# Optimization experiments

Hardware: AMD Instinct MI355X
Metric: run time of the kernel (lower is better)

The kernel has to match this reference:

```python
import jax, jax.numpy as jnp
import numpy as np

V, E_DIM, HID, GNN_O, HEADS = 50257, 256, 128, 128, 4
N_NODES, N_EDGES, T_LEN = 10000, 160000, 64
NEG_SLOPE = 0.2


def gatv2(x, src, dst, Wl, Wr, att, bias, concat):
    """PyG GATv2Conv (share_weights=False, self-loops already in src/dst)."""
    heads, out_ch = att.shape
    n = x.shape[0]
    xl = (x @ Wl).reshape(n, heads, out_ch)   # source transform
    xr = (x @ Wr).reshape(n, heads, out_ch)   # target transform
    e = jax.nn.leaky_relu(xl[src] + xr[dst], NEG_SLOPE)        # [E, h, c]
    logits = jnp.einsum('ehc,hc->eh', e, att)                  # [E, h]
    m = jax.ops.segment_max(logits, dst, num_segments=n)
    a = jnp.exp(logits - m[dst])
    a = a / jax.ops.segment_sum(a, dst, num_segments=n)[dst]
    out = jax.ops.segment_sum(xl[src] * a[..., None], dst, num_segments=n)
    out = out.reshape(n, heads * out_ch) if concat else out.mean(axis=1)
    return out + bias


def setup_inputs() -> dict:
    key = jax.random.key(0)
    ks = jax.random.split(key, 16)
    g = lambda k, shape: jax.random.normal(k, shape, jnp.float32) * 0.05
    x_nodes = jax.random.randint(ks[0], (N_NODES,), 0, V)
    edge_index = jax.random.randint(ks[1], (2, N_EDGES), 0, N_NODES)
    target_sequence = jax.random.randint(ks[2], (1, T_LEN), 0, V)
    return dict(
        x_nodes=x_nodes, edge_index=edge_index, target_sequence=target_sequence,
        embedding=g(ks[3], (V, E_DIM)),
        W1l=g(ks[4], (E_DIM, HEADS * HID)), W1r=g(ks[5], (E_DIM, HEADS * HID)),
        att1=g(ks[6], (HEADS, HID)), b1=jnp.zeros((HEADS * HID,), jnp.float32),
        W2l=g(ks[7], (HEADS * HID, GNN_O)), W2r=g(ks[8], (HEADS * HID, GNN_O)),
        att2=g(ks[9], (1, GNN_O)), b2=jnp.zeros((GNN_O,), jnp.float32),
        Wih=g(ks[10], (3 * HID, GNN_O + E_DIM)), Whh=g(ks[11], (3 * HID, HID)),
        bih=jnp.zeros((3 * HID,), jnp.float32), bhh=jnp.zeros((3 * HID,), jnp.float32),
        Wout=g(ks[12], (V, HID)), bout=jnp.zeros((V,), jnp.float32),
    )


def reference(x_nodes, edge_index, target_sequence, embedding,
              W1l, W1r, att1, b1, W2l, W2r, att2, b2,
              Wih, Whh, bih, bhh, Wout, bout):
    n = x_nodes.shape[0]
    loops = jnp.arange(n, dtype=edge_index.dtype)
    src = jnp.concatenate([edge_index[0], loops])   # add self-loops (PyG default)
    dst = jnp.concatenate([edge_index[1], loops])
    feats = embedding[x_nodes]                      # [N, E_DIM] (dropout off: eval)
    h1 = jax.nn.elu(gatv2(feats, src, dst, W1l, W1r, att1, b1, concat=True))
    enc = gatv2(h1, src, dst, W2l, W2r, att2, b2, concat=False)  # [N, GNN_O]
    context = enc.mean(axis=0)                      # constant across decode steps

    # teacher forcing (ratio=1.0): input tokens are SOS(0) then shifted targets
    tokens = jnp.concatenate([jnp.zeros((1,), target_sequence.dtype),
                              target_sequence[0, :-1]])

    def step(h, tok):
        x = jnp.concatenate([embedding[tok], context])          # [E_DIM+GNN_O]
        gi = Wih @ x + bih
        gh = Whh @ h + bhh
        ir, iz, inn = jnp.split(gi, 3)
        hr, hz, hn = jnp.split(gh, 3)
        r = jax.nn.sigmoid(ir + hr)
        z = jax.nn.sigmoid(iz + hz)
        cand = jnp.tanh(inn + r * hn)
        h_new = (1.0 - z) * cand + z * h
        logits = Wout @ h_new + bout
        return h_new, logits

    h0 = jnp.zeros((Whh.shape[1],), jnp.float32)
    _, logits = jax.lax.scan(step, h0, tokens)      # [T, V]
    return logits[None]                              # [1, T, V]
```

## Files before the change

kernel.cpp:

```cpp
#include <hip/hip_runtime.h>
#include <hip/hip_bf16.h>
#include <math.h>

#define NNODES 10000
#define NEDGES 160000
#define EDIM   256
#define HIDC   128
#define TLEN   64
#define VOCAB  50257
#define NEG    0.2f

typedef __bf16 bf16x8 __attribute__((ext_vector_type(8)));
typedef float  f32x4  __attribute__((ext_vector_type(4)));
typedef unsigned short u16x8 __attribute__((ext_vector_type(8)));

static __device__ __forceinline__ float leaky(float x){ return x > 0.f ? x : NEG*x; }
static __device__ __forceinline__ float sigm (float x){ return __fdividef(1.f, 1.f + __expf(-x)); }
static __device__ __forceinline__ float eluf (float x){ return x > 0.f ? x : expm1f(x); }
static __device__ __forceinline__ unsigned short bf16rn(float f){
  unsigned a = __float_as_uint(f);
  return (unsigned short)((a + 0x7FFFu + ((a >> 16) & 1u)) >> 16);
}
static __device__ __forceinline__ float upf(unsigned short u){ return __uint_as_float(((unsigned)u) << 16); }

__global__ void k_featsb(const int* __restrict__ xn, const float* __restrict__ emb,
                         unsigned short* __restrict__ featsb){
  int node = blockIdx.x*4 + (threadIdx.x >> 6);
  int l = threadIdx.x & 63;
  float4 v = ((const float4*)(emb + (size_t)xn[node]*EDIM))[l];
  ushort4 o; o.x = bf16rn(v.x); o.y = bf16rn(v.y); o.z = bf16rn(v.z); o.w = bf16rn(v.w);
  *(ushort4*)(featsb + (size_t)node*EDIM + 4*l) = o;
}

__global__ void k_wcast(const float* __restrict__ in, unsigned short* __restrict__ out, int n4){
  int idx = blockIdx.x*256 + threadIdx.x;
  if (idx < n4){
    float4 v = ((const float4*)in)[idx];
    ushort4 o; o.x = bf16rn(v.x); o.y = bf16rn(v.y); o.z = bf16rn(v.z); o.w = bf16rn(v.w);
    ((ushort4*)out)[idx] = o;
  }
}

__global__ __launch_bounds__(256) void k_tr(const float* __restrict__ in,
    unsigned short* __restrict__ out, int K, int Nin)
{
  __shared__ unsigned short tile[64][72];
  int k0 = blockIdx.x*64, n0 = blockIdx.y*64;
  int t = threadIdx.x;
  int tr = t >> 4, tc4 = (t & 15)*4;
  #pragma unroll
  for (int it = 0; it < 4; ++it){
    int kr = tr + 16*it;
    float4 v = *(const float4*)(in + (size_t)(k0+kr)*Nin + n0 + tc4);
    tile[tc4+0][kr] = bf16rn(v.x);
    tile[tc4+1][kr] = bf16rn(v.y);
    tile[tc4+2][kr] = bf16rn(v.z);
    tile[tc4+3][kr] = bf16rn(v.w);
  }
  __syncthreads();
  #pragma unroll
  for (int it = 0; it < 4; ++it){
    int nr = tr + 16*it;
    ushort4 o;
    o.x = tile[nr][tc4+0]; o.y = tile[nr][tc4+1];
    o.z = tile[nr][tc4+2]; o.w = tile[nr][tc4+3];
    *(ushort4*)(out + (size_t)(n0+nr)*K + k0 + tc4) = o;
  }
}

__global__ void k_deg(const int* __restrict__ dst, int* __restrict__ deg){
  int e = blockIdx.x*256 + threadIdx.x;
  if (e < NEDGES) atomicAdd(&deg[dst[e]], 1);
}

__global__ __launch_bounds__(1024) void k_scan(const int* __restrict__ deg, int* __restrict__ offs){
  __shared__ int s[1024];
  int t = threadIdx.x;
  int loc[10]; int sum = 0;
  #pragma unroll
  for (int q = 0; q < 10; q++){
    int idx = t*10 + q;
    loc[q] = sum;
    sum += (idx < NNODES) ? deg[idx] : 0;
  }
  s[t] = sum;
  __syncthreads();
  for (int ofs = 1; ofs < 1024; ofs <<= 1){
    int v = (t >= ofs) ? s[t-ofs] : 0;
    __syncthreads();
    s[t] += v;
    __syncthreads();
  }
  int pre = (t > 0) ? s[t-1] : 0;
  #pragma unroll
  for (int q = 0; q < 10; q++){
    int idx = t*10 + q;
    if (idx < NNODES) offs[idx] = pre + loc[q];
  }
  if (t == 1023) offs[NNODES] = s[1023];
}

__global__ void k_scatter(const int* __restrict__ src, const int* __restrict__ dst,
                          const int* __restrict__ offs, int* __restrict__ cursor,
                          int* __restrict__ esrc){
  int e = blockIdx.x*256 + threadIdx.x;
  if (e >= NEDGES) return;
  int d = dst[e];
  int p = atomicAdd(&cursor[d], 1);
  esrc[offs[d] + p] = src[e];
}

template<int KDIM>
__global__ __launch_bounds__(256) void k_mfma(const unsigned short* __restrict__ A,
    const unsigned short* __restrict__ Bt, unsigned short* __restrict__ C,
    int M, int N)
{
  __shared__ __align__(16) unsigned short As[128*64];
  __shared__ __align__(16) unsigned short Bs[128*64];
  int tid = threadIdx.x;
  int l   = tid & 63;
  int wid = tid >> 6;
  int wr = wid >> 1, wc = wid & 1;
  int row0 = blockIdx.x * 128, col0 = blockIdx.y * 128;
  int lr = l & 15, kg = l >> 4;
  f32x4 acc[4][4] = {};

  for (int kt = 0; kt < KDIM/64; ++kt){
    int k0 = kt*64;
    #pragma unroll
    for (int c = 0; c < 4; ++c){
      int chunk = wid*4 + c;
      int arow = row0 + chunk*8 + (l >> 3);
      if (arow > M-1) arow = M-1;
      const unsigned short* ga = A + (size_t)arow*KDIM + k0 + (l & 7)*8;
      __builtin_amdgcn_global_load_lds(
          (const __attribute__((address_space(1))) void*)ga,
          (__attribute__((address_space(3))) void*)(As + chunk*512), 16, 0, 0);
      int brow = col0 + chunk*8 + (l >> 3);
      const unsigned short* gb = Bt + (size_t)brow*KDIM + k0 + (l & 7)*8;
      __builtin_amdgcn_global_load_lds(
          (const __attribute__((address_space(1))) void*)gb,
          (__attribute__((address_space(3))) void*)(Bs + chunk*512), 16, 0, 0);
    }
    __syncthreads();
    #pragma unroll
    for (int ks = 0; ks < 2; ++ks){
      bf16x8 af[4], bfr[4];
      #pragma unroll
      for (int m = 0; m < 4; ++m)
        af[m] = *(const bf16x8*)(As + (wr*64 + m*16 + lr)*64 + ks*32 + kg*8);
      #pragma unroll
      for (int n = 0; n < 4; ++n)
        bfr[n] = *(const bf16x8*)(Bs + (wc*64 + n*16 + lr)*64 + ks*32 + kg*8);
      #pragma unroll
      for (int m = 0; m < 4; ++m)
        #pragma unroll
        for (int n = 0; n < 4; ++n)
          acc[m][n] = __builtin_amdgcn_mfma_f32_16x16x32_bf16(af[m], bfr[n], acc[m][n], 0, 0, 0);
    }
    __syncthreads();
  }

  #pragma unroll
  for (int m = 0; m < 4; ++m){
    int rbase = row0 + wr*64 + m*16 + kg*4;
    #pragma unroll
    for (int r = 0; r < 4; ++r){
      int row = rbase + r;
      if (row < M){
        #pragma unroll
        for (int n = 0; n < 4; ++n){
          int col = col0 + wc*64 + n*16 + lr;
          C[(size_t)row*N + col] = bf16rn(acc[m][n][r]);
        }
      }
    }
  }
}

__global__ __launch_bounds__(256) void k_mout(const unsigned short* __restrict__ A,
    const unsigned short* __restrict__ Bt, const float* __restrict__ bias,
    float* __restrict__ out)
{
  __shared__ __align__(16) unsigned short As[64*128];
  __shared__ __align__(16) unsigned short Bs[128*128];
  int tid = threadIdx.x;
  int l   = tid & 63;
  int wid = tid >> 6;
  int col0 = blockIdx.x * 128;
  int lr = l & 15, kg = l >> 4;

  #pragma unroll
  for (int c = 0; c < 4; ++c){
    int chunk = wid*4 + c;
    const unsigned short* ga = A + (size_t)(chunk*4 + (l >> 4))*128 + (l & 15)*8;
    __builtin_amdgcn_global_load_lds(
        (const __attribute__((address_space(1))) void*)ga,
        (__attribute__((address_space(3))) void*)(As + chunk*512), 16, 0, 0);
  }
  #pragma unroll
  for (int c = 0; c < 8; ++c){
    int chunk = wid*8 + c;
    int brow = col0 + chunk*4 + (l >> 4);
    if (brow > VOCAB-1) brow = VOCAB-1;
    const unsigned short* gb = Bt + (size_t)brow*128 + (l & 15)*8;
    __builtin_amdgcn_global_load_lds(
        (const __attribute__((address_space(1))) void*)gb,
        (__attribute__((address_space(3))) void*)(Bs + chunk*512), 16, 0, 0);
  }
  __syncthreads();

  f32x4 acc[4][2] = {};
  #pragma unroll
  for (int ks = 0; ks < 4; ++ks){
    bf16x8 af[4], bfr[2];
    #pragma unroll
    for (int m = 0; m < 4; ++m)
      af[m] = *(const bf16x8*)(As + (m*16 + lr)*128 + ks*32 + kg*8);
    #pragma unroll
    for (int n = 0; n < 2; ++n)
      bfr[n] = *(const bf16x8*)(Bs + (wid*32 + n*16 + lr)*128 + ks*32 + kg*8);
    #pragma unroll
    for (int m = 0; m < 4; ++m)
      #pragma unroll
      for (int n = 0; n < 2; ++n)
        acc[m][n] = __builtin_amdgcn_mfma_f32_16x16x32_bf16(af[m], bfr[n], acc[m][n], 0, 0, 0);
  }

  #pragma unroll
  for (int n = 0; n < 2; ++n){
    int col = col0 + wid*32 + n*16 + lr;
    if (col < VOCAB){
      float bv = bias[col];
      #pragma unroll
      for (int m = 0; m < 4; ++m){
        #pragma unroll
        for (int r = 0; r < 4; ++r){
          int trow = m*16 + kg*4 + r;
          out[(size_t)trow*VOCAB + col] = acc[m][n][r] + bv;
        }
      }
    }
  }
}

__global__ __launch_bounds__(256) void k_gat1(const unsigned short* __restrict__ xlr,
    const int* __restrict__ esrc, const int* __restrict__ offs,
    const float* __restrict__ att, const float* __restrict__ b1,
    unsigned short* __restrict__ h1b)
{
  int node = blockIdx.x*4 + (threadIdx.x >> 6);
  int l = threadIdx.x & 63;
  const unsigned short* bi = xlr + (size_t)node*1024;
  ushort4 u;
  u = *(const ushort4*)(bi + 512 + 4*l);
  float4 xr1; xr1.x = upf(u.x); xr1.y = upf(u.y); xr1.z = upf(u.z); xr1.w = upf(u.w);
  u = *(const ushort4*)(bi + 768 + 4*l);
  float4 xr2; xr2.x = upf(u.x); xr2.y = upf(u.y); xr2.z = upf(u.z); xr2.w = upf(u.w);
  int hq = l >> 5;
  float4 at1 = *(const float4*)(att + hq*HIDC + ((4*l) & 127));
  float4 at2 = *(const float4*)(att + (2+hq)*HIDC + ((4*l) & 127));
  float4 ac1 = {0,0,0,0}, ac2 = {0,0,0,0};
  float d1 = 0.f, d2 = 0.f;
  int beg = offs[node], end = offs[node+1];
  for (int p = beg-1; p < end; ++p){
    int s = (p < beg) ? node : esrc[p];
    const unsigned short* bs = xlr + (size_t)s*1024;
    ushort4 u1 = *(const ushort4*)(bs + 4*l);
    ushort4 u2 = *(const ushort4*)(bs + 256 + 4*l);
    float4 x1; x1.x = upf(u1.x); x1.y = upf(u1.y); x1.z = upf(u1.z); x1.w = upf(u1.w);
    float4 x2; x2.x = upf(u2.x); x2.y = upf(u2.y); x2.z = upf(u2.z); x2.w = upf(u2.w);
    float p1 = leaky(x1.x+xr1.x)*at1.x + leaky(x1.y+xr1.y)*at1.y
             + leaky(x1.z+xr1.z)*at1.z + leaky(x1.w+xr1.w)*at1.w;
    float p2 = leaky(x2.x+xr2.x)*at2.x + leaky(x2.y+xr2.y)*at2.y
             + leaky(x2.z+xr2.z)*at2.z + leaky(x2.w+xr2.w)*at2.w;
    #pragma unroll
    for (int m = 1; m <= 16; m <<= 1){
      p1 += __shfl_xor(p1, m);
      p2 += __shfl_xor(p2, m);
    }
    float w1 = __expf(p1), w2 = __expf(p2);
    ac1.x = fmaf(w1, x1.x, ac1.x); ac1.y = fmaf(w1, x1.y, ac1.y);
    ac1.z = fmaf(w1, x1.z, ac1.z); ac1.w = fmaf(w1, x1.w, ac1.w);
    ac2.x = fmaf(w2, x2.x, ac2.x); ac2.y = fmaf(w2, x2.y, ac2.y);
    ac2.z = fmaf(w2, x2.z, ac2.z); ac2.w = fmaf(w2, x2.w, ac2.w);
    d1 += w1; d2 += w2;
  }
  float i1 = 1.f/d1, i2 = 1.f/d2;
  const float* bq1 = b1 + 4*l;
  const float* bq2 = b1 + 256 + 4*l;
  ushort4 o1, o2;
  o1.x = bf16rn(eluf(ac1.x*i1 + bq1[0])); o1.y = bf16rn(eluf(ac1.y*i1 + bq1[1]));
  o1.z = bf16rn(eluf(ac1.z*i1 + bq1[2])); o1.w = bf16rn(eluf(ac1.w*i1 + bq1[3]));
  o2.x = bf16rn(eluf(ac2.x*i2 + bq2[0])); o2.y = bf16rn(eluf(ac2.y*i2 + bq2[1]));
  o2.z = bf16rn(eluf(ac2.z*i2 + bq2[2])); o2.w = bf16rn(eluf(ac2.w*i2 + bq2[3]));
  *(ushort4*)(h1b + (size_t)node*512 + 4*l)       = o1;
  *(ushort4*)(h1b + (size_t)node*512 + 256 + 4*l) = o2;
}

__global__ __launch_bounds__(256) void k_gat2(const unsigned short* __restrict__ xlr2,
    const int* __restrict__ esrc, const int* __restrict__ offs,
    const float* __restrict__ att2, const float* __restrict__ b2,
    float* __restrict__ enc)
{
  int node = blockIdx.x*4 + (threadIdx.x >> 6);
  int l = threadIdx.x & 63;
  const unsigned short* bi = xlr2 + (size_t)node*256;
  ushort2 v = *(const ushort2*)(bi + 128 + 2*l);
  float2 xr; xr.x = upf(v.x); xr.y = upf(v.y);
  float2 at = *(const float2*)(att2 + 2*l);
  float2 ac = {0,0}; float den = 0.f;
  int beg = offs[node], end = offs[node+1];
  for (int p = beg-1; p < end; ++p){
    int s = (p < beg) ? node : esrc[p];
    ushort2 xv = *(const ushort2*)(xlr2 + (size_t)s*256 + 2*l);
    float2 x; x.x = upf(xv.x); x.y = upf(xv.y);
    float pp = leaky(x.x+xr.x)*at.x + leaky(x.y+xr.y)*at.y;
    #pragma unroll
    for (int m = 1; m <= 32; m <<= 1) pp += __shfl_xor(pp, m);
    float w = __expf(pp);
    ac.x = fmaf(w, x.x, ac.x); ac.y = fmaf(w, x.y, ac.y);
    den += w;
  }
  float inv = 1.f/den;
  float2 o; o.x = ac.x*inv + b2[2*l]; o.y = ac.y*inv + b2[2*l+1];
  *(float2*)(enc + (size_t)node*128 + 2*l) = o;
}

__global__ void k_mean(const float* __restrict__ enc, float* __restrict__ ctx){
  int c = threadIdx.x & 127;
  int slice = blockIdx.x*2 + (threadIdx.x >> 7);
  float s = 0.f;
  for (int i = slice; i < NNODES; i += 160) s += enc[(size_t)i*128 + c];
  atomicAdd(&ctx[c], s * (1.f/NNODES));
}

__global__ __launch_bounds__(384) void k_gi(const int* __restrict__ tseq,
    const float* __restrict__ emb, const float* __restrict__ ctx,
    const float* __restrict__ Wih, const float* __restrict__ bih,
    float* __restrict__ Gi)
{
  __shared__ float xs[384];
  int t = blockIdx.x, tid = threadIdx.x;
  int tok = (t == 0) ? 0 : tseq[t-1];
  if (tid < 256) xs[tid] = emb[(size_t)tok*EDIM + tid];
  else           xs[tid] = ctx[tid - 256];
  __syncthreads();
  const float* w = Wih + (size_t)tid*384;
  float acc = bih[tid];
  #pragma unroll 8
  for (int k = 0; k < 384; k++) acc = fmaf(w[k], xs[k], acc);
  Gi[t*384 + tid] = acc;
}

__global__ __launch_bounds__(384) void k_gru(const float* __restrict__ Gi,
    const float* __restrict__ Whh, const float* __restrict__ bhh,
    unsigned short* __restrict__ HTt)
{
  __shared__ float GH[384];
  __shared__ __align__(16) unsigned short hhi[128];
  __shared__ __align__(16) unsigned short hlo[128];
  int tid = threadIdx.x;
  int l = tid & 63, w = tid >> 6;
  int lr = l & 15, kg = l >> 4;

  bf16x8 afr[4][4];
  #pragma unroll
  for (int t4 = 0; t4 < 4; ++t4){
    int row = w*64 + t4*16 + lr;
    const float* rp = Whh + (size_t)row*HIDC;
    #pragma unroll
    for (int ks = 0; ks < 4; ++ks){
      const float* p = rp + ks*32 + kg*8;
      float4 v0 = *(const float4*)p;
      float4 v1 = *(const float4*)(p + 4);
      u16x8 u;
      u[0] = bf16rn(v0.x); u[1] = bf16rn(v0.y); u[2] = bf16rn(v0.z); u[3] = bf16rn(v0.w);
      u[4] = bf16rn(v1.x); u[5] = bf16rn(v1.y); u[6] = bf16rn(v1.z); u[7] = bf16rn(v1.w);
      afr[t4][ks] = __builtin_bit_cast(bf16x8, u);
    }
  }

  float bh0 = 0.f, bh1 = 0.f, bh2 = 0.f, hloc = 0.f;
  if (tid < 128){
    bh0 = bhh[tid];
    bh1 = bhh[128 + tid];
    bh2 = bhh[256 + tid];
    hhi[tid] = 0; hlo[tid] = 0;
  }
  __syncthreads();

  for (int t = 0; t < TLEN; t++){
    float gi0 = 0.f, gi1 = 0.f, gi2 = 0.f;
    if (tid < 128){
      gi0 = Gi[t*384 + tid];
      gi1 = Gi[t*384 + 128 + tid];
      gi2 = Gi[t*384 + 256 + tid];
    }
    bf16x8 bhi[4], blo[4];
    #pragma unroll
    for (int ks = 0; ks < 4; ++ks){
      bhi[ks] = *(const bf16x8*)(hhi + ks*32 + kg*8);
      blo[ks] = *(const bf16x8*)(hlo + ks*32 + kg*8);
    }
    f32x4 acc[4] = {};
    #pragma unroll
    for (int ks = 0; ks < 4; ++ks){
      #pragma unroll
      for (int t4 = 0; t4 < 4; ++t4){
        acc[t4] = __builtin_amdgcn_mfma_f32_16x16x32_bf16(afr[t4][ks], bhi[ks], acc[t4], 0, 0, 0);
        acc[t4] = __builtin_amdgcn_mfma_f32_16x16x32_bf16(afr[t4][ks], blo[ks], acc[t4], 0, 0, 0);
      }
    }
    if (lr == 0){
      #pragma unroll
      for (int t4 = 0; t4 < 4; ++t4){
        *(f32x4*)&GH[w*64 + t4*16 + kg*4] = acc[t4];
      }
    }
    __syncthreads();
    if (tid < 128){
      float gr = gi0 + GH[tid]       + bh0;
      float gz = gi1 + GH[128 + tid] + bh1;
      float hn = GH[256 + tid]       + bh2;
      float r = sigm(gr);
      float z = sigm(gz);
      float e2 = __expf(2.f*(gi2 + r*hn));
      float cand = __fdividef(e2 - 1.f, e2 + 1.f);
      float hnew = (1.f - z)*cand + z*hloc;
      hloc = hnew;
      unsigned short hi = bf16rn(hnew);
      hhi[tid] = hi;
      hlo[tid] = bf16rn(hnew - upf(hi));
      HTt[t*HIDC + tid] = hi;
    }
    __syncthreads();
  }
}

extern "C" void kernel_launch(void* const* d_in, const int* in_sizes, int n_in,
                              void* d_out, int out_size, void* d_ws, size_t ws_size,
                              hipStream_t stream)
{
  const int*   x_nodes = (const int*)  d_in[0];
  const int*   eidx    = (const int*)  d_in[1];
  const int*   tseq    = (const int*)  d_in[2];
  const float* emb     = (const float*)d_in[3];
  const float* W1l     = (const float*)d_in[4];
  const float* W1r     = (const float*)d_in[5];
  const float* att1    = (const float*)d_in[6];
  const float* b1      = (const float*)d_in[7];
  const float* W2l     = (const float*)d_in[8];
  const float* W2r     = (const float*)d_in[9];
  const float* att2    = (const float*)d_in[10];
  const float* b2      = (const float*)d_in[11];
  const float* Wih     = (const float*)d_in[12];
  const float* Whh     = (const float*)d_in[13];
  const float* bih     = (const float*)d_in[14];
  const float* bhh     = (const float*)d_in[15];
  const float* Wout    = (const float*)d_in[16];
  const float* bout    = (const float*)d_in[17];
  float* out = (float*)d_out;
  char*  ws  = (char*)d_ws;

  unsigned short* xlr1b  = (unsigned short*)(ws);
  unsigned short* h1b    = (unsigned short*)(ws + 20480000);
  unsigned short* featsb = (unsigned short*)(ws + 30720000);
  unsigned short* xlr2b  = (unsigned short*)(ws + 35840000);
  float*          enc    = (float*)        (ws + 40960000);
  unsigned short* Bt1    = (unsigned short*)(ws + 46080000);
  unsigned short* Bt2    = (unsigned short*)(ws + 46604288);
  int*   deg    = (int*)(ws + 46866432);
  int*   offs   = (int*)(ws + 46906432);
  int*   cursor = (int*)(ws + 46946436);
  int*   esrc   = (int*)(ws + 46986436);
  float* ctx    = (float*)(ws + 47626440);
  float* Gi     = (float*)(ws + 47627008);
  unsigned short* HTt   = (unsigned short*)(ws + 47725312);
  unsigned short* Woutb = (unsigned short*)(ws + 47741696);

  hipMemsetAsync(deg,    0, NNODES*sizeof(int), stream);
  hipMemsetAsync(cursor, 0, NNODES*sizeof(int), stream);

  k_featsb<<<2500, 256, 0, stream>>>(x_nodes, emb, featsb);
  k_wcast <<<6283, 256, 0, stream>>>(Wout, Woutb, VOCAB*128/4);
  k_tr<<<dim3(4,8), 256, 0, stream>>>(W1l, Bt1,            256, 512);
  k_tr<<<dim3(4,8), 256, 0, stream>>>(W1r, Bt1 + 512*256,  256, 512);
  k_tr<<<dim3(8,2), 256, 0, stream>>>(W2l, Bt2,            512, 128);
  k_tr<<<dim3(8,2), 256, 0, stream>>>(W2r, Bt2 + 128*512,  512, 128);

  k_deg    <<<625, 256, 0, stream>>>(eidx + NEDGES, deg);
  k_scan   <<<1,  1024, 0, stream>>>(deg, offs);
  k_scatter<<<625, 256, 0, stream>>>(eidx, eidx + NEDGES, offs, cursor, esrc);

  k_mfma<256><<<dim3(79,8), 256, 0, stream>>>(featsb, Bt1, xlr1b, NNODES, 1024);
  k_gat1<<<2500, 256, 0, stream>>>(xlr1b, esrc, offs, att1, b1, h1b);

  k_mfma<512><<<dim3(79,2), 256, 0, stream>>>(h1b, Bt2, xlr2b, NNODES, 256);
  k_gat2<<<2500, 256, 0, stream>>>(xlr2b, esrc, offs, att2, b2, enc);

  hipMemsetAsync(ctx, 0, 128*sizeof(float), stream);
  k_mean<<<80, 256, 0, stream>>>(enc, ctx);
  k_gi  <<<TLEN, 384, 0, stream>>>(tseq, emb, ctx, Wih, bih, Gi);
  k_gru <<<1, 384, 0, stream>>>(Gi, Whh, bhh, HTt);

  k_mout<<<393, 256, 0, stream>>>(HTt, Woutb, bout, out);
}
```

Measured before the change: 289.2 us.

## Fuse GRU gate math into MFMA lanes with double-buffered hidden state

Each wave now owns 32 hidden units across all three gates, so the r/z/n gate math runs directly on the MFMA accumulator registers. This removes the shared GH staging array and one of the two barriers per timestep. The hidden state is double-buffered in shared memory so writers and readers never overlap, and the block shrinks from 384 to 256 threads. The tradeoff is more registers per thread and redundant gate math across lanes (every lane computes it, only lr==0 writes).

```diff
diff --git a/kernel.cpp b/kernel.cpp
--- a/kernel.cpp
+++ b/kernel.cpp
@@ -353,86 +353,96 @@
   Gi[t*384 + tid] = acc;
 }
 
-__global__ __launch_bounds__(384) void k_gru(const float* __restrict__ Gi,
+__global__ __launch_bounds__(256) void k_gru(const float* __restrict__ Gi,
     const float* __restrict__ Whh, const float* __restrict__ bhh,
     unsigned short* __restrict__ HTt)
 {
-  __shared__ float GH[384];
-  __shared__ __align__(16) unsigned short hhi[128];
-  __shared__ __align__(16) unsigned short hlo[128];
+  __shared__ __align__(16) unsigned short hbuf[2][2][128];
   int tid = threadIdx.x;
   int l = tid & 63, w = tid >> 6;
   int lr = l & 15, kg = l >> 4;
 
-  bf16x8 afr[4][4];
-  #pragma unroll
-  for (int t4 = 0; t4 < 4; ++t4){
-    int row = w*64 + t4*16 + lr;
-    const float* rp = Whh + (size_t)row*HIDC;
+  bf16x8 afr[3][2][4];
+  float  bh [3][2][4];
+  #pragma unroll
+  for (int g = 0; g < 3; ++g){
+    #pragma unroll
+    for (int s = 0; s < 2; ++s){
+      int row = g*128 + w*32 + s*16 + lr;
+      const float* rp = Whh + (size_t)row*HIDC;
+      #pragma unroll
+      for (int ks = 0; ks < 4; ++ks){
+        const float* p = rp + ks*32 + kg*8;
+        float4 v0 = *(const float4*)p;
+        float4 v1 = *(const float4*)(p + 4);
+        u16x8 u;
+        u[0] = bf16rn(v0.x); u[1] = bf16rn(v0.y); u[2] = bf16rn(v0.z); u[3] = bf16rn(v0.w);
+        u[4] = bf16rn(v1.x); u[5] = bf16rn(v1.y); u[6] = bf16rn(v1.z); u[7] = bf16rn(v1.w);
+        afr[g][s][ks] = __builtin_bit_cast(bf16x8, u);
+      }
+      int rb = g*128 + w*32 + s*16 + kg*4;
+      #pragma unroll
+      for (int r = 0; r < 4; ++r) bh[g][s][r] = bhh[rb + r];
+    }
+  }
+
+  float hloc[2][4] = {};
+  if (tid < 128){ hbuf[0][0][tid] = 0; hbuf[0][1][tid] = 0; }
+  __syncthreads();
+
+  for (int t = 0; t < TLEN; t++){
+    f32x4 gi[3][2];
+    #pragma unroll
+    for (int g = 0; g < 3; ++g)
+      #pragma unroll
+      for (int s = 0; s < 2; ++s)
+        gi[g][s] = *(const f32x4*)(Gi + t*384 + g*128 + w*32 + s*16 + kg*4);
+
+    int rb = t & 1, wb = rb ^ 1;
+    bf16x8 bhi[4], blo[4];
     #pragma unroll
     for (int ks = 0; ks < 4; ++ks){
-      const float* p = rp + ks*32 + kg*8;
-      float4 v0 = *(const float4*)p;
-      float4 v1 = *(const float4*)(p + 4);
-      u16x8 u;
-      u[0] = bf16rn(v0.x); u[1] = bf16rn(v0.y); u[2] = bf16rn(v0.z); u[3] = bf16rn(v0.w);
-      u[4] = bf16rn(v1.x); u[5] = bf16rn(v1.y); u[6] = bf16rn(v1.z); u[7] = bf16rn(v1.w);
-      afr[t4][ks] = __builtin_bit_cast(bf16x8, u);
-    }
-  }
-
-  float bh0 = 0.f, bh1 = 0.f, bh2 = 0.f, hloc = 0.f;
-  if (tid < 128){
-    bh0 = bhh[tid];
-    bh1 = bhh[128 + tid];
-    bh2 = bhh[256 + tid];
-    hhi[tid] = 0; hlo[tid] = 0;
-  }
-  __syncthreads();
-
-  for (int t = 0; t < TLEN; t++){
-    float gi0 = 0.f, gi1 = 0.f, gi2 = 0.f;
-    if (tid < 128){
-      gi0 = Gi[t*384 + tid];
-      gi1 = Gi[t*384 + 128 + tid];
-      gi2 = Gi[t*384 + 256 + tid];
-    }
-    bf16x8 bhi[4], blo[4];
+      bhi[ks] = *(const bf16x8*)(&hbuf[rb][0][ks*32 + kg*8]);
+      blo[ks] = *(const bf16x8*)(&hbuf[rb][1][ks*32 + kg*8]);
+    }
+    f32x4 acc[3][2] = {};
     #pragma unroll
     for (int ks = 0; ks < 4; ++ks){
-      bhi[ks] = *(const bf16x8*)(hhi + ks*32 + kg*8);
-      blo[ks] = *(const bf16x8*)(hlo + ks*32 + kg*8);
-    }
-    f32x4 acc[4] = {};
-    #pragma unroll
-    for (int ks = 0; ks < 4; ++ks){
-      #pragma unroll
-      for (int t4 = 0; t4 < 4; ++t4){
-        acc[t4] = __builtin_amdgcn_mfma_f32_16x16x32_bf16(afr[t4][ks], bhi[ks], acc[t4], 0, 0, 0);
-        acc[t4] = __builtin_amdgcn_mfma_f32_16x16x32_bf16(afr[t4][ks], blo[ks], acc[t4], 0, 0, 0);
+      #pragma unroll
+      for (int g = 0; g < 3; ++g){
+        #pragma unroll
+        for (int s = 0; s < 2; ++s){
+          acc[g][s] = __builtin_amdgcn_mfma_f32_16x16x32_bf16(afr[g][s][ks], bhi[ks], acc[g][s], 0, 0, 0);
+          acc[g][s] = __builtin_amdgcn_mfma_f32_16x16x32_bf16(afr[g][s][ks], blo[ks], acc[g][s], 0, 0, 0);
+        }
       }
     }
-    if (lr == 0){
-      #pragma unroll
-      for (int t4 = 0; t4 < 4; ++t4){
-        *(f32x4*)&GH[w*64 + t4*16 + kg*4] = acc[t4];
+    #pragma unroll
+    for (int s = 0; s < 2; ++s){
+      ushort4 hi4, lo4;
+      unsigned short hv[4], lv[4];
+      #pragma unroll
+      for (int r = 0; r < 4; ++r){
+        float gr = gi[0][s][r] + acc[0][s][r] + bh[0][s][r];
+        float gz = gi[1][s][r] + acc[1][s][r] + bh[1][s][r];
+        float hn = acc[2][s][r] + bh[2][s][r];
+        float rr = sigm(gr);
+        float z  = sigm(gz);
+        float e2 = __expf(2.f*(gi[2][s][r] + rr*hn));
+        float cand = __fdividef(e2 - 1.f, e2 + 1.f);
+        float hnew = (1.f - z)*cand + z*hloc[s][r];
+        hloc[s][r] = hnew;
+        hv[r] = bf16rn(hnew);
+        lv[r] = bf16rn(hnew - upf(hv[r]));
       }
-    }
-    __syncthreads();
-    if (tid < 128){
-      float gr = gi0 + GH[tid]       + bh0;
-      float gz = gi1 + GH[128 + tid] + bh1;
-      float hn = GH[256 + tid]       + bh2;
-      float r = sigm(gr);
-      float z = sigm(gz);
-      float e2 = __expf(2.f*(gi2 + r*hn));
-      float cand = __fdividef(e2 - 1.f, e2 + 1.f);
-      float hnew = (1.f - z)*cand + z*hloc;
-      hloc = hnew;
-      unsigned short hi = bf16rn(hnew);
-      hhi[tid] = hi;
-      hlo[tid] = bf16rn(hnew - upf(hi));
-      HTt[t*HIDC + tid] = hi;
+      hi4.x = hv[0]; hi4.y = hv[1]; hi4.z = hv[2]; hi4.w = hv[3];
+      lo4.x = lv[0]; lo4.y = lv[1]; lo4.z = lv[2]; lo4.w = lv[3];
+      if (lr == 0){
+        int row0 = w*32 + s*16 + kg*4;
+        *(ushort4*)(&hbuf[wb][0][row0]) = hi4;
+        *(ushort4*)(&hbuf[wb][1][row0]) = lo4;
+        *(ushort4*)(HTt + t*HIDC + row0) = hi4;
+      }
     }
     __syncthreads();
   }
@@ -502,7 +512,7 @@
   hipMemsetAsync(ctx, 0, 128*sizeof(float), stream);
   k_mean<<<80, 256, 0, stream>>>(enc, ctx);
   k_gi  <<<TLEN, 384, 0, stream>>>(tseq, emb, ctx, Wih, bih, Gi);
-  k_gru <<<1, 384, 0, stream>>>(Gi, Whh, bhh, HTt);
+  k_gru <<<1, 256, 0, stream>>>(Gi, Whh, bhh, HTt);
 
   k_mout<<<393, 256, 0, stream>>>(HTt, Woutb, bout, out);
 }
```

New measurement: 327.8 us. +13.3%, slower.
